# Kernel optimization log

Hardware: AMD Instinct MI355X
Metric: run time of the kernel (lower is better)

The kernel has to match this reference:

```python
import jax, jax.numpy as jnp
import numpy as np

H = 64      # hidden_dimension
NH = 4      # num_heads
L = 2       # num_egat_layers
N = 20000   # total nodes in batched graph
E = 320000  # total edges
B = 64      # number of graphs in batch
SLOPE = 0.2 # DGL EGATConv leaky_relu negative slope


def setup_inputs() -> dict:
    key = jax.random.key(0)
    ks = iter(jax.random.split(key, 40))
    def nrm(shape, scale=0.05):
        return jax.random.normal(next(ks), shape, dtype=jnp.float32) * scale
    node_graph_id = jnp.sort(jax.random.randint(next(ks), (N,), 0, B))
    src = jax.random.randint(next(ks), (E,), 0, N)
    dst = jax.random.randint(next(ks), (E,), 0, N)
    edge_graph_id = node_graph_id[dst]
    return dict(
        x=nrm((N, 81), 1.0), e=nrm((E, 17), 1.0),
        placed_rc=jax.random.randint(next(ks), (N,), 0, 2),
        fp=nrm((B, 2048), 1.0),
        src=src, dst=dst, node_graph_id=node_graph_id, edge_graph_id=edge_graph_id,
        W_fp=nrm((2048, H)), b_fp=jnp.zeros((H,), jnp.float32),
        W_n0=nrm((81, H)), b_n0=jnp.zeros((H,), jnp.float32),
        W_e0=nrm((17, H)), b_e0=jnp.zeros((H,), jnp.float32),
        emb_rc=nrm((2, H)),
        fc_node_W=nrm((L, H, NH * H)), fc_ni_W=nrm((L, H, NH * H)),
        fc_nj_W=nrm((L, H, NH * H)), fc_fij_W=nrm((L, H, NH * H)),
        attn=nrm((L, NH, H)), egat_bias=jnp.zeros((L, NH * H), jnp.float32),
        mlp_n_W=nrm((L, NH * H, H)), mlp_n_b=jnp.zeros((L, H), jnp.float32),
        mlp_e_W=nrm((L, NH * H, H)), mlp_e_b=jnp.zeros((L, H), jnp.float32),
        W_g=nrm((3 * H, H)), b_g=jnp.zeros((H,), jnp.float32),
    )


def _egat_layer(nf, ef, src, dst, p):
    # One EGATLayer: DGL EGATConv + per-output MLP + ELU.
    fcnW, fniW, fnjW, ffW, attn, ebias, mnW, mnb, meW, meb = p
    f_out = nf[src] @ fniW + nf[dst] @ fnjW + ef @ ffW          # [E, NH*H]
    f_out = jax.nn.leaky_relu(f_out, SLOPE).reshape(E, NH, H)    # [E, NH, H]
    logits = jnp.einsum('ehd,hd->eh', f_out, attn)               # [E, NH]
    # edge softmax over incoming edges at each destination node
    m = jax.ops.segment_max(logits, dst, num_segments=N)
    ex = jnp.exp(logits - m[dst])
    denom = jax.ops.segment_sum(ex, dst, num_segments=N)
    a = ex / denom[dst]                                          # [E, NH]
    h = (nf @ fcnW).reshape(N, NH, H)                            # [N, NH, H]
    msg = h[src] * a[..., None]                                  # [E, NH, H]
    h_out = jax.ops.segment_sum(msg, dst, num_segments=N)        # [N, NH, H]
    h_out = h_out + ebias.reshape(NH, H)[None]
    new_n = jax.nn.elu(h_out.reshape(N, NH * H) @ mnW + mnb)     # [N, H]
    new_e = jax.nn.elu(f_out.reshape(E, NH * H) @ meW + meb)     # [E, H]
    return new_n, new_e


def reference(x, e, placed_rc, fp, src, dst, node_graph_id, edge_graph_id,
              W_fp, b_fp, W_n0, b_n0, W_e0, b_e0, emb_rc,
              fc_node_W, fc_ni_W, fc_nj_W, fc_fij_W, attn, egat_bias,
              mlp_n_W, mlp_n_b, mlp_e_W, mlp_e_b, W_g, b_g):
    fp_enc = jax.nn.elu(fp @ W_fp + b_fp)                        # [B, H]
    nf = x @ W_n0 + b_n0 + emb_rc[placed_rc]                     # [N, H]
    ef = e @ W_e0 + b_e0                                         # [E, H]
    for l in range(L):  # residual EGAT stack
        rn, re = nf, ef
        nf, ef = _egat_layer(nf, ef, src, dst,
            (fc_node_W[l], fc_ni_W[l], fc_nj_W[l], fc_fij_W[l], attn[l],
             egat_bias[l], mlp_n_W[l], mlp_n_b[l], mlp_e_W[l], mlp_e_b[l]))
        nf = nf + rn
        ef = ef + re
    # mean readout per graph
    cnt_n = jax.ops.segment_sum(jnp.ones((N,), jnp.float32), node_graph_id, num_segments=B)
    cnt_e = jax.ops.segment_sum(jnp.ones((E,), jnp.float32), edge_graph_id, num_segments=B)
    g_n = jax.ops.segment_sum(nf, node_graph_id, num_segments=B) / jnp.maximum(cnt_n, 1.0)[:, None]
    g_e = jax.ops.segment_sum(ef, edge_graph_id, num_segments=B) / jnp.maximum(cnt_e, 1.0)[:, None]
    g = jnp.concatenate([g_n, g_e, fp_enc], axis=1)              # [B, 3H]
    g = jax.nn.elu(g @ W_g + b_g)                                # [B, H]
    return nf, g
```

## Files before the change

### kernel.cpp

```cpp
#include <hip/hip_runtime.h>
#include <math.h>

#define SLOPE 0.2f

typedef __attribute__((ext_vector_type(8))) short bf16x8;
typedef __attribute__((ext_vector_type(4))) float f32x4;

__device__ __forceinline__ unsigned short f2bf(float x) {
  unsigned int b = __float_as_uint(x);
  b = (b + 0x7fffu + ((b >> 16) & 1u)) >> 16;
  return (unsigned short)b;
}
__device__ __forceinline__ float bf2f(unsigned short u) {
  return __uint_as_float(((unsigned int)u) << 16);
}
__device__ __forceinline__ float elu1(float v) { return v > 0.f ? v : expm1f(v); }
__device__ __forceinline__ float lrelu(float v) { return v > 0.f ? v : SLOPE * v; }

__global__ __launch_bounds__(256) void k_zero(float* p, long n) {
  long i = (long)blockIdx.x * 256 + threadIdx.x;
  long stride = (long)gridDim.x * 256;
  for (; i < n; i += stride) p[i] = 0.f;
}

__global__ __launch_bounds__(256) void k_fp(const float* __restrict__ fp,
                                            const float* __restrict__ W,
                                            float* __restrict__ fpacc) {
  __shared__ float red[256];
  const int b = blockIdx.x >> 3;
  const int kc = blockIdx.x & 7;
  const int t = threadIdx.x, o = t & 63, kg = t >> 6;
  const int k0 = kc * 256 + kg * 64;
  const float* fpr = fp + (size_t)b * 2048 + k0;
  const float* Wp = W + (size_t)k0 * 64 + o;
  float a0 = 0.f, a1 = 0.f, a2 = 0.f, a3 = 0.f;
#pragma unroll
  for (int i = 0; i < 64; i += 4) {
    a0 += fpr[i + 0] * Wp[(i + 0) * 64];
    a1 += fpr[i + 1] * Wp[(i + 1) * 64];
    a2 += fpr[i + 2] * Wp[(i + 2) * 64];
    a3 += fpr[i + 3] * Wp[(i + 3) * 64];
  }
  red[t] = (a0 + a1) + (a2 + a3);
  __syncthreads();
  if (t < 64) {
    float v = red[t] + red[t + 64] + red[t + 128] + red[t + 192];
    atomicAdd(&fpacc[(size_t)b * 64 + t], v);
  }
}

__global__ __launch_bounds__(256) void k_nf0(const float* __restrict__ x,
                                             const float* __restrict__ W,
                                             const float* __restrict__ bias,
                                             const float* __restrict__ emb,
                                             const int* __restrict__ prc,
                                             float* __restrict__ nf,
                                             unsigned short* __restrict__ nfB, int N) {
  __shared__ float xl[64 * 85];
  const int t = threadIdx.x, l = t & 63, q = t >> 6;
  const int nbase = blockIdx.x * 64;
  const long xbase = (long)nbase * 81;
  const long xlim = (long)N * 81;
  for (int i = t; i < 5184; i += 256) {
    int row = i / 81, k = i - row * 81;
    float v = (xbase + i < xlim) ? x[xbase + i] : 0.f;
    xl[row * 85 + k] = v;
  }
  __syncthreads();
  const int n = nbase + l;
  const int nc = n < N ? n : N - 1;
  const int o0 = q * 16;
  const int pv = prc[nc];
  float acc[16];
#pragma unroll
  for (int i = 0; i < 16; ++i) acc[i] = bias[o0 + i] + emb[pv * 64 + o0 + i];
  for (int k = 0; k < 81; ++k) {
    float xv = xl[l * 85 + k];
    float w[16];
    const float4* wp = (const float4*)(W + (long)k * 64 + o0);
    *(float4*)&w[0] = wp[0]; *(float4*)&w[4] = wp[1];
    *(float4*)&w[8] = wp[2]; *(float4*)&w[12] = wp[3];
#pragma unroll
    for (int i = 0; i < 16; ++i) acc[i] += xv * w[i];
  }
  if (n < N) {
#pragma unroll
    for (int u = 0; u < 4; ++u)
      *(float4*)(nf + (long)n * 64 + o0 + 4 * u) =
          make_float4(acc[4 * u], acc[4 * u + 1], acc[4 * u + 2], acc[4 * u + 3]);
    unsigned pk[8];
#pragma unroll
    for (int u = 0; u < 8; ++u)
      pk[u] = (unsigned)f2bf(acc[2 * u]) | ((unsigned)f2bf(acc[2 * u + 1]) << 16);
    *(uint4*)(nfB + (size_t)n * 64 + o0) = make_uint4(pk[0], pk[1], pk[2], pk[3]);
    *(uint4*)(nfB + (size_t)n * 64 + o0 + 8) = make_uint4(pk[4], pk[5], pk[6], pk[7]);
  }
}

__global__ __launch_bounds__(256) void k_ef0(const float* __restrict__ ein,
                                             const int* __restrict__ eids,
                                             const float* __restrict__ W,
                                             const float* __restrict__ bias,
                                             unsigned short* __restrict__ efB, int E) {
  const int t = threadIdx.x, l = t & 63, q = t >> 6;
  const long i = (long)blockIdx.x * 64 + l;
  const long ic = i < E ? i : 0;
  const long e = eids[ic];
  const int o0 = q * 16;
  float acc[16];
#pragma unroll
  for (int k = 0; k < 16; ++k) acc[k] = bias[o0 + k];
  for (int k = 0; k < 17; ++k) {
    float xv = ein[e * 17 + k];
    float w[16];
    const float4* wp = (const float4*)(W + (long)k * 64 + o0);
    *(float4*)&w[0] = wp[0]; *(float4*)&w[4] = wp[1];
    *(float4*)&w[8] = wp[2]; *(float4*)&w[12] = wp[3];
#pragma unroll
    for (int u = 0; u < 16; ++u) acc[u] += xv * w[u];
  }
  if (i < E) {
    unsigned pk[8];
#pragma unroll
    for (int u = 0; u < 8; ++u)
      pk[u] = (unsigned)f2bf(acc[2 * u]) | ((unsigned)f2bf(acc[2 * u + 1]) << 16);
    *(uint4*)(efB + i * 64 + o0) = make_uint4(pk[0], pk[1], pk[2], pk[3]);
    *(uint4*)(efB + i * 64 + o0 + 8) = make_uint4(pk[4], pk[5], pk[6], pk[7]);
  }
}

__global__ __launch_bounds__(256) void k_hist(const int* __restrict__ dst, int* deg, int E) {
  int e = blockIdx.x * 256 + threadIdx.x;
  if (e < E) atomicAdd(&deg[dst[e]], 1);
}

__global__ __launch_bounds__(1024) void k_scan(const int* __restrict__ deg, int* rowst,
                                               int* cursor, int N, int E) {
  __shared__ int s[1024];
  const int t = threadIdx.x;
  const int CH = (N + 1023) / 1024;
  const int base = t * CH;
  int sum = 0;
  for (int i = 0; i < CH; ++i) { int n = base + i; if (n < N) sum += deg[n]; }
  s[t] = sum;
  __syncthreads();
  for (int off = 1; off < 1024; off <<= 1) {
    int v = (t >= off) ? s[t - off] : 0;
    __syncthreads();
    s[t] += v;
    __syncthreads();
  }
  int run = s[t] - sum;
  for (int i = 0; i < CH; ++i) {
    int n = base + i;
    if (n < N) { rowst[n] = run; cursor[n] = run; run += deg[n]; }
  }
  if (t == 1023) rowst[N] = E;
}

__global__ __launch_bounds__(256) void k_fill(const int* __restrict__ dst,
                                              const int* __restrict__ src,
                                              const int* __restrict__ egid,
                                              int* cursor, int* eids,
                                              int* srcC, int* dstC, int* egidC, int E) {
  int e = blockIdx.x * 256 + threadIdx.x;
  if (e < E) {
    int d = dst[e];
    int pos = atomicAdd(&cursor[d], 1);
    eids[pos] = e;
    srcC[pos] = src[e];
    dstC[pos] = d;
    egidC[pos] = egid[e];
  }
}

__global__ __launch_bounds__(256) void k_pack(const float* __restrict__ fni,
                                              const float* __restrict__ fnj,
                                              const float* __restrict__ ffij,
                                              const float* __restrict__ meW,
                                              unsigned short* __restrict__ pA,
                                              unsigned short* __restrict__ pB) {
  int t = blockIdx.x * 256 + threadIdx.x;
  if (t < 6144) {
    int lane = t & 63;
    int ks = (t >> 6) % 6;
    int nt = t / 384;
    int n = nt * 16 + (lane & 15);
    int kbase = ks * 32 + (lane >> 4) * 8;
    bf16x8 v;
#pragma unroll
    for (int j = 0; j < 8; ++j) {
      int kk = kbase + j;
      float wv = kk < 64 ? fni[kk * 256 + n]
                         : (kk < 128 ? fnj[(kk - 64) * 256 + n] : ffij[(kk - 128) * 256 + n]);
      v[j] = (short)f2bf(wv);
    }
    *(bf16x8*)(pA + (size_t)t * 8) = v;
  } else if (t < 8192) {
    int u = t - 6144;
    int lane = u & 63;
    int ks = (u >> 6) % 8;
    int nt = u / 512;
    int n = nt * 16 + (lane & 15);
    int kbase = ks * 32 + (lane >> 4) * 8;
    bf16x8 v;
#pragma unroll
    for (int j = 0; j < 8; ++j) v[j] = (short)f2bf(meW[(size_t)(kbase + j) * 64 + n]);
    *(bf16x8*)(pB + (size_t)u * 8) = v;
  }
}

__global__ __launch_bounds__(256) void k_comb(const float* __restrict__ fcn,
                                              const float* __restrict__ mnW,
                                              const float* __restrict__ mnb,
                                              const float* __restrict__ ebias,
                                              float* __restrict__ Wcomb,
                                              float* __restrict__ bprime) {
  const int b = blockIdx.x, t = threadIdx.x;
  if (b < 4) {
    const int h = b, i = t & 63, c0 = (t >> 6) * 16;
    float acc[16];
#pragma unroll
    for (int c = 0; c < 16; ++c) acc[c] = 0.f;
    for (int j = 0; j < 64; ++j) {
      float w1 = fcn[i * 256 + h * 64 + j];
      const float4* mp = (const float4*)(mnW + (size_t)(h * 64 + j) * 64 + c0);
      float mw[16];
      *(float4*)&mw[0] = mp[0]; *(float4*)&mw[4] = mp[1];
      *(float4*)&mw[8] = mp[2]; *(float4*)&mw[12] = mp[3];
#pragma unroll
      for (int c = 0; c < 16; ++c) acc[c] += w1 * mw[c];
    }
    for (int c = 0; c < 16; ++c) Wcomb[(size_t)(h * 64 + i) * 64 + c0 + c] = acc[c];
  } else {
    if (t < 64) {
      float a = mnb[t];
      for (int k = 0; k < 256; ++k) a += ebias[k] * mnW[(size_t)k * 64 + t];
      bprime[t] = a;
    }
  }
}

__global__ __launch_bounds__(256) void k_packB(const float* __restrict__ W,
                                               unsigned short* __restrict__ dst) {
  int u = blockIdx.x * 256 + threadIdx.x;
  if (u >= 2048) return;
  int lane = u & 63;
  int ks = (u >> 6) % 8;
  int nt = u / 512;
  int n = nt * 16 + (lane & 15);
  int kbase = ks * 32 + (lane >> 4) * 8;
  bf16x8 v;
#pragma unroll
  for (int j = 0; j < 8; ++j) v[j] = (short)f2bf(W[(size_t)(kbase + j) * 64 + n]);
  *(bf16x8*)(dst + (size_t)u * 8) = v;
}

__global__ __launch_bounds__(256, 4) void k_edge(const unsigned short* __restrict__ nfB,
                                                 const unsigned short* __restrict__ efB,
                                                 const unsigned short* __restrict__ pA,
                                                 const unsigned short* __restrict__ pB,
                                                 const float* __restrict__ attnW,
                                                 const float* __restrict__ meb,
                                                 const int* __restrict__ srcC,
                                                 const int* __restrict__ dstC,
                                                 unsigned short* __restrict__ efBout,
                                                 float* __restrict__ logitsC,
                                                 const int* __restrict__ egidC,
                                                 float* __restrict__ geOut,
                                                 float* __restrict__ ceOut, int E) {
  __shared__ __align__(16) char smem[32768 + 1024 + 512];
  float* lgx = (float*)(smem + 32768);
  int* sv = (int*)(smem + 32768 + 1024);
  int* dv = (int*)(smem + 32768 + 1024 + 256);
  const int t = threadIdx.x, l = t & 63, w = t >> 6;
  const long ebase = (long)blockIdx.x * 64;

  if (t < 64) sv[t] = srcC[min(ebase + t, (long)E - 1)];
  else if (t < 128) dv[t - 64] = dstC[min(ebase + t - 64, (long)E - 1)];
  __syncthreads();
#pragma unroll
  for (int i = 0; i < 6; ++i) {
    int c = i * 256 + t;
    int row = c / 24;
    int kc8 = c - row * 24;
    long e = ebase + row;
    if (e >= E) e = E - 1;
    int ko = (kc8 & 7) * 8;
    int seg = kc8 >> 3;
    const unsigned short* gp;
    if (seg == 0)      gp = nfB + (size_t)sv[row] * 64 + ko;
    else if (seg == 1) gp = nfB + (size_t)dv[row] * 64 + ko;
    else               gp = efB + (size_t)e * 64 + ko;
    uint4 v = *(const uint4*)gp;
    *(uint4*)(smem + row * 384 + ((kc8 * 16) ^ ((row & 7) << 4))) = v;
  }
  __syncthreads();

  f32x4 acc[4][4];
#pragma unroll
  for (int c0 = 0; c0 < 4; ++c0)
#pragma unroll
    for (int e0 = 0; e0 < 4; ++e0) acc[c0][e0] = (f32x4){0.f, 0.f, 0.f, 0.f};

  for (int ks = 0; ks < 6; ++ks) {
    bf16x8 eb[4], wa[4];
#pragma unroll
    for (int e0 = 0; e0 < 4; ++e0) {
      int row = e0 * 16 + (l & 15);
      int kb = ks * 64 + (l >> 4) * 16;
      eb[e0] = *(const bf16x8*)(smem + row * 384 + (kb ^ ((row & 7) << 4)));
    }
#pragma unroll
    for (int c0 = 0; c0 < 4; ++c0)
      wa[c0] = *(const bf16x8*)(pA + (size_t)(((w * 4 + c0) * 6 + ks) * 64 + l) * 8);
#pragma unroll
    for (int c0 = 0; c0 < 4; ++c0)
#pragma unroll
      for (int e0 = 0; e0 < 4; ++e0)
        acc[c0][e0] = __builtin_amdgcn_mfma_f32_16x16x32_bf16(wa[c0], eb[e0], acc[c0][e0], 0, 0, 0);
  }
  __syncthreads();

  float avv[4][4];
#pragma unroll
  for (int c0 = 0; c0 < 4; ++c0) {
    float4 a4 = *(const float4*)(attnW + w * 64 + c0 * 16 + (l >> 4) * 4);
    avv[c0][0] = a4.x; avv[c0][1] = a4.y; avv[c0][2] = a4.z; avv[c0][3] = a4.w;
  }
  float lgp[4] = {0.f, 0.f, 0.f, 0.f};
#pragma unroll
  for (int e0 = 0; e0 < 4; ++e0) {
    int row = e0 * 16 + (l & 15);
#pragma unroll
    for (int c0 = 0; c0 < 4; ++c0) {
      float v0 = lrelu(acc[c0][e0][0]);
      float v1 = lrelu(acc[c0][e0][1]);
      float v2 = lrelu(acc[c0][e0][2]);
      float v3 = lrelu(acc[c0][e0][3]);
      lgp[e0] += v0 * avv[c0][0] + v1 * avv[c0][1] + v2 * avv[c0][2] + v3 * avv[c0][3];
      uint2 p;
      p.x = (unsigned)f2bf(v0) | ((unsigned)f2bf(v1) << 16);
      p.y = (unsigned)f2bf(v2) | ((unsigned)f2bf(v3) << 16);
      int colb = (w * 64 + c0 * 16 + (l >> 4) * 4) * 2;
      *(uint2*)(smem + row * 512 + (colb ^ ((row & 7) << 4))) = p;
    }
  }
#pragma unroll
  for (int e0 = 0; e0 < 4; ++e0) {
    float v = lgp[e0];
    v += __shfl_xor(v, 16);
    v += __shfl_xor(v, 32);
    if (l < 16) lgx[(e0 * 16 + l) * 4 + w] = v;
  }
  __syncthreads();

  if (t < 64) {
    long e = ebase + t;
    if (e < E) *(float4*)(logitsC + e * 4) = *(const float4*)(lgx + t * 4);
  }

  f32x4 a2[4];
#pragma unroll
  for (int e0 = 0; e0 < 4; ++e0) a2[e0] = (f32x4){0.f, 0.f, 0.f, 0.f};
  for (int ks = 0; ks < 8; ++ks) {
    bf16x8 fb[4];
#pragma unroll
    for (int e0 = 0; e0 < 4; ++e0) {
      int row = e0 * 16 + (l & 15);
      int kb = ks * 64 + (l >> 4) * 16;
      fb[e0] = *(const bf16x8*)(smem + row * 512 + (kb ^ ((row & 7) << 4)));
    }
    bf16x8 pb = *(const bf16x8*)(pB + (size_t)((w * 8 + ks) * 64 + l) * 8);
#pragma unroll
    for (int e0 = 0; e0 < 4; ++e0)
      a2[e0] = __builtin_amdgcn_mfma_f32_16x16x32_bf16(pb, fb[e0], a2[e0], 0, 0, 0);
  }
  const int cb = w * 16 + (l >> 4) * 4;
  float4 mb4 = *(const float4*)(meb + cb);
  __syncthreads();
#pragma unroll
  for (int e0 = 0; e0 < 4; ++e0) {
    int row = e0 * 16 + (l & 15);
    float4 o;
    o.x = elu1(a2[e0][0] + mb4.x);
    o.y = elu1(a2[e0][1] + mb4.y);
    o.z = elu1(a2[e0][2] + mb4.z);
    o.w = elu1(a2[e0][3] + mb4.w);
    *(float4*)(smem + (size_t)(row * 68 + cb) * 4) = o;
  }
  __syncthreads();
#pragma unroll
  for (int i = 0; i < 4; ++i) {
    int idx = i * 256 + t;
    int row = idx >> 4;
    int c4 = (idx & 15) * 4;
    long e = ebase + row;
    if (e < E) {
      uint2 rb = *(const uint2*)(efB + e * 64 + c4);
      float4 v = *(const float4*)(smem + (size_t)(row * 68 + c4) * 4);
      v.x += bf2f((unsigned short)(rb.x & 0xffffu));
      v.y += bf2f((unsigned short)(rb.x >> 16));
      v.z += bf2f((unsigned short)(rb.y & 0xffffu));
      v.w += bf2f((unsigned short)(rb.y >> 16));
      if (efBout) {
        uint2 ob;
        ob.x = (unsigned)f2bf(v.x) | ((unsigned)f2bf(v.y) << 16);
        ob.y = (unsigned)f2bf(v.z) | ((unsigned)f2bf(v.w) << 16);
        *(uint2*)(efBout + e * 64 + c4) = ob;
      }
      if (geOut) *(float4*)(smem + (size_t)(row * 68 + c4) * 4) = v;
    }
  }
  if (geOut) {
    if (t < 64) sv[t] = (ebase + t < E) ? egidC[ebase + t] : -1;
    __syncthreads();
    if (t < 64) {
      int nrows = (int)min((long)64, E - ebase);
      float racc = 0.f, cnt = 0.f;
      int curg = sv[0];
      for (int r = 0; r < nrows; ++r) {
        int g = sv[r];
        if (g != curg) {
          atomicAdd(&geOut[(size_t)curg * 64 + t], racc);
          if (t == 0) atomicAdd(&ceOut[curg], cnt);
          racc = 0.f; cnt = 0.f; curg = g;
        }
        racc += *(const float*)(smem + (size_t)(r * 68 + t) * 4);
        cnt += 1.f;
      }
      if (curg >= 0) {
        atomicAdd(&geOut[(size_t)curg * 64 + t], racc);
        if (t == 0) atomicAdd(&ceOut[curg], cnt);
      }
    }
  }
}

__global__ __launch_bounds__(256) void k_node(const float* __restrict__ logitsC,
                                              const unsigned short* __restrict__ nfB,
                                              const int* __restrict__ rowst,
                                              const int* __restrict__ srcC,
                                              unsigned short* __restrict__ agg, int N) {
  const int t = threadIdx.x, w = t >> 6, l = t & 63;
  const int n = blockIdx.x * 4 + w;
  if (n >= N) return;
  const int start = rowst[n];
  const int dg = rowst[n + 1] - start;
  const int h = l >> 4;
  float m0 = -INFINITY, m1 = -INFINITY, m2 = -INFINITY, m3 = -INFINITY;
  for (int base = 0; base < dg; base += 64) {
    int j = base + l;
    if (j < dg) {
      float4 lg = *(const float4*)(logitsC + (long)(start + j) * 4);
      m0 = fmaxf(m0, lg.x); m1 = fmaxf(m1, lg.y); m2 = fmaxf(m2, lg.z); m3 = fmaxf(m3, lg.w);
    }
  }
#pragma unroll
  for (int o = 1; o < 64; o <<= 1) {
    m0 = fmaxf(m0, __shfl_xor(m0, o)); m1 = fmaxf(m1, __shfl_xor(m1, o));
    m2 = fmaxf(m2, __shfl_xor(m2, o)); m3 = fmaxf(m3, __shfl_xor(m3, o));
  }
  const float msel = (h == 0) ? m0 : (h == 1) ? m1 : (h == 2) ? m2 : m3;

  const int co = (l & 15) * 4;
  float s = 0.f;
  float a0 = 0.f, a1 = 0.f, a2 = 0.f, a3 = 0.f;
  int j = 0;
  for (; j + 4 <= dg; j += 4) {
    int sj0 = srcC[start + j + 0];
    int sj1 = srcC[start + j + 1];
    int sj2 = srcC[start + j + 2];
    int sj3 = srcC[start + j + 3];
    float l0 = logitsC[(long)(start + j + 0) * 4 + h];
    float l1 = logitsC[(long)(start + j + 1) * 4 + h];
    float l2 = logitsC[(long)(start + j + 2) * 4 + h];
    float l3 = logitsC[(long)(start + j + 3) * 4 + h];
    uint2 b0 = *(const uint2*)(nfB + (size_t)sj0 * 64 + co);
    uint2 b1 = *(const uint2*)(nfB + (size_t)sj1 * 64 + co);
    uint2 b2 = *(const uint2*)(nfB + (size_t)sj2 * 64 + co);
    uint2 b3 = *(const uint2*)(nfB + (size_t)sj3 * 64 + co);
    float aa0 = __expf(l0 - msel);
    float aa1 = __expf(l1 - msel);
    float aa2 = __expf(l2 - msel);
    float aa3 = __expf(l3 - msel);
    s += (aa0 + aa1) + (aa2 + aa3);
    a0 += aa0 * bf2f((unsigned short)(b0.x & 0xffffu)) + aa1 * bf2f((unsigned short)(b1.x & 0xffffu))
        + aa2 * bf2f((unsigned short)(b2.x & 0xffffu)) + aa3 * bf2f((unsigned short)(b3.x & 0xffffu));
    a1 += aa0 * bf2f((unsigned short)(b0.x >> 16)) + aa1 * bf2f((unsigned short)(b1.x >> 16))
        + aa2 * bf2f((unsigned short)(b2.x >> 16)) + aa3 * bf2f((unsigned short)(b3.x >> 16));
    a2 += aa0 * bf2f((unsigned short)(b0.y & 0xffffu)) + aa1 * bf2f((unsigned short)(b1.y & 0xffffu))
        + aa2 * bf2f((unsigned short)(b2.y & 0xffffu)) + aa3 * bf2f((unsigned short)(b3.y & 0xffffu));
    a3 += aa0 * bf2f((unsigned short)(b0.y >> 16)) + aa1 * bf2f((unsigned short)(b1.y >> 16))
        + aa2 * bf2f((unsigned short)(b2.y >> 16)) + aa3 * bf2f((unsigned short)(b3.y >> 16));
  }
  for (; j < dg; ++j) {
    int sj = srcC[start + j];
    float lg = logitsC[(long)(start + j) * 4 + h];
    float a = __expf(lg - msel);
    s += a;
    uint2 b0 = *(const uint2*)(nfB + (size_t)sj * 64 + co);
    a0 += a * bf2f((unsigned short)(b0.x & 0xffffu));
    a1 += a * bf2f((unsigned short)(b0.x >> 16));
    a2 += a * bf2f((unsigned short)(b0.y & 0xffffu));
    a3 += a * bf2f((unsigned short)(b0.y >> 16));
  }
  const float rsel = (dg > 0) ? (1.f / s) : 0.f;
  a0 *= rsel; a1 *= rsel; a2 *= rsel; a3 *= rsel;
  unsigned v0 = (unsigned)f2bf(a0) | ((unsigned)f2bf(a1) << 16);
  unsigned v1 = (unsigned)f2bf(a2) | ((unsigned)f2bf(a3) << 16);
  uint2 vv; vv.x = v0; vv.y = v1;
  *(uint2*)(agg + (size_t)n * 256 + h * 64 + co) = vv;
}

__global__ __launch_bounds__(256, 4) void k_mlpn(const unsigned short* __restrict__ agg,
                                                 const unsigned short* __restrict__ pW,
                                                 const float* __restrict__ bprime,
                                                 float* __restrict__ nf,
                                                 unsigned short* __restrict__ nfB,
                                                 float* __restrict__ dout,
                                                 const int* __restrict__ ngid,
                                                 float* __restrict__ gnOut,
                                                 float* __restrict__ cnOut, int N) {
  __shared__ __align__(16) char sm[64 * 512];
  __shared__ int gidL[64];
  const int t = threadIdx.x, l = t & 63, w = t >> 6;
  const int nbase = blockIdx.x * 64;
#pragma unroll
  for (int i = 0; i < 8; ++i) {
    int idx = t + 256 * i;
    int row = idx >> 5, kc = idx & 31;
    int rr = (nbase + row) < N ? (nbase + row) : (N - 1);
    uint4 v = *(const uint4*)(agg + (size_t)rr * 256 + kc * 8);
    *(uint4*)(sm + row * 512 + ((kc * 16) ^ ((row & 7) << 4))) = v;
  }
  __syncthreads();
  f32x4 acc[4];
#pragma unroll
  for (int e0 = 0; e0 < 4; ++e0) acc[e0] = (f32x4){0.f, 0.f, 0.f, 0.f};
  for (int ks = 0; ks < 8; ++ks) {
    bf16x8 a[4];
#pragma unroll
    for (int e0 = 0; e0 < 4; ++e0) {
      int row = e0 * 16 + (l & 15);
      int kb = ks * 64 + (l >> 4) * 16;
      a[e0] = *(const bf16x8*)(sm + row * 512 + (kb ^ ((row & 7) << 4)));
    }
    bf16x8 b = *(const bf16x8*)(pW + (size_t)((w * 8 + ks) * 64 + l) * 8);
#pragma unroll
    for (int e0 = 0; e0 < 4; ++e0)
      acc[e0] = __builtin_amdgcn_mfma_f32_16x16x32_bf16(b, a[e0], acc[e0], 0, 0, 0);
  }
  const int cb = w * 16 + (l >> 4) * 4;
  float4 bp4 = *(const float4*)(bprime + cb);
  __syncthreads();
#pragma unroll
  for (int e0 = 0; e0 < 4; ++e0) {
    int row = e0 * 16 + (l & 15);
    float4 o;
    o.x = elu1(acc[e0][0] + bp4.x);
    o.y = elu1(acc[e0][1] + bp4.y);
    o.z = elu1(acc[e0][2] + bp4.z);
    o.w = elu1(acc[e0][3] + bp4.w);
    *(float4*)(sm + (size_t)(row * 68 + cb) * 4) = o;
  }
  if (gnOut && t < 64) gidL[t] = (nbase + t < N) ? ngid[nbase + t] : -1;
  __syncthreads();
#pragma unroll
  for (int i = 0; i < 4; ++i) {
    int idx = i * 256 + t;
    int row = idx >> 4;
    int c4 = (idx & 15) * 4;
    int n = nbase + row;
    if (n < N) {
      float4 res = *(const float4*)(nf + (size_t)n * 64 + c4);
      float4 v = *(const float4*)(sm + (size_t)(row * 68 + c4) * 4);
      v.x += res.x; v.y += res.y; v.z += res.z; v.w += res.w;
      *(float4*)(nf + (size_t)n * 64 + c4) = v;
      uint2 ob;
      ob.x = (unsigned)f2bf(v.x) | ((unsigned)f2bf(v.y) << 16);
      ob.y = (unsigned)f2bf(v.z) | ((unsigned)f2bf(v.w) << 16);
      *(uint2*)(nfB + (size_t)n * 64 + c4) = ob;
      if (dout) *(float4*)(dout + (size_t)n * 64 + c4) = v;
      if (gnOut) *(float4*)(sm + (size_t)(row * 68 + c4) * 4) = v;
    }
  }
  if (gnOut) {
    __syncthreads();
    if (t < 64) {
      int nrows = min(64, N - nbase);
      float racc = 0.f, cnt = 0.f;
      int curg = gidL[0];
      for (int r = 0; r < nrows; ++r) {
        int g = gidL[r];
        if (g != curg) {
          atomicAdd(&gnOut[(size_t)curg * 64 + t], racc);
          if (t == 0) atomicAdd(&cnOut[curg], cnt);
          racc = 0.f; cnt = 0.f; curg = g;
        }
        racc += *(const float*)(sm + (size_t)(r * 68 + t) * 4);
        cnt += 1.f;
      }
      if (curg >= 0) {
        atomicAdd(&gnOut[(size_t)curg * 64 + t], racc);
        if (t == 0) atomicAdd(&cnOut[curg], cnt);
      }
    }
  }
}

__global__ __launch_bounds__(64) void k_final(const float* __restrict__ gn,
                                              const float* __restrict__ ge,
                                              const float* __restrict__ cntn,
                                              const float* __restrict__ cnte,
                                              const float* __restrict__ fpacc,
                                              const float* __restrict__ bfp,
                                              const float* __restrict__ Wg,
                                              const float* __restrict__ bg,
                                              float* __restrict__ outg) {
  __shared__ float gv[192];
  const int b = blockIdx.x, l = threadIdx.x;
  const float rn = 1.f / fmaxf(cntn[b], 1.f);
  const float re = 1.f / fmaxf(cnte[b], 1.f);
  gv[l] = gn[(long)b * 64 + l] * rn;
  gv[64 + l] = ge[(long)b * 64 + l] * re;
  gv[128 + l] = elu1(fpacc[(long)b * 64 + l] + bfp[l]);
  __syncthreads();
  float acc = bg[l];
  for (int k = 0; k < 192; ++k) acc += gv[k] * Wg[(long)k * 64 + l];
  outg[(long)b * 64 + l] = elu1(acc);
}

extern "C" void kernel_launch(void* const* d_in, const int* in_sizes, int n_in,
                              void* d_out, int out_size, void* d_ws, size_t ws_size,
                              hipStream_t stream) {
  (void)n_in; (void)out_size; (void)ws_size;
  const float* x       = (const float*)d_in[0];
  const float* ein     = (const float*)d_in[1];
  const int*   prc     = (const int*)d_in[2];
  const float* fp      = (const float*)d_in[3];
  const int*   src     = (const int*)d_in[4];
  const int*   dst     = (const int*)d_in[5];
  const int*   ngid    = (const int*)d_in[6];
  const int*   egid    = (const int*)d_in[7];
  const float* W_fp    = (const float*)d_in[8];
  const float* b_fp    = (const float*)d_in[9];
  const float* W_n0    = (const float*)d_in[10];
  const float* b_n0    = (const float*)d_in[11];
  const float* W_e0    = (const float*)d_in[12];
  const float* b_e0    = (const float*)d_in[13];
  const float* emb_rc  = (const float*)d_in[14];
  const float* fc_node = (const float*)d_in[15];
  const float* fc_ni   = (const float*)d_in[16];
  const float* fc_nj   = (const float*)d_in[17];
  const float* fc_fij  = (const float*)d_in[18];
  const float* attnp   = (const float*)d_in[19];
  const float* egb     = (const float*)d_in[20];
  const float* mlp_n_W = (const float*)d_in[21];
  const float* mlp_n_b = (const float*)d_in[22];
  const float* mlp_e_W = (const float*)d_in[23];
  const float* mlp_e_b = (const float*)d_in[24];
  const float* W_g     = (const float*)d_in[25];
  const float* b_g     = (const float*)d_in[26];

  const int N = in_sizes[0] / 81;
  const int E = in_sizes[1] / 17;
  const int B = in_sizes[3] / 2048;
  float* out = (float*)d_out;

  char* ws = (char*)d_ws;
  size_t off = 0;
  auto carve = [&](size_t bytes) {
    size_t r = off;
    off = (off + bytes + 255) & ~(size_t)255;
    return r;
  };
  size_t o_nf   = carve((size_t)N * 64 * 4);
  size_t o_nfB  = carve((size_t)N * 64 * 2);
  size_t o_efB  = carve((size_t)E * 64 * 2);
  size_t o_agg  = carve((size_t)N * 256 * 2);
  size_t o_lg   = carve((size_t)E * 4 * 4);
  size_t o_pA   = carve((size_t)2 * 6144 * 8 * 2);
  size_t o_pB   = carve((size_t)2 * 2048 * 8 * 2);
  size_t o_Wc   = carve((size_t)2 * 256 * 64 * 4);
  size_t o_pW   = carve((size_t)2 * 2048 * 8 * 2);
  size_t o_bp   = carve((size_t)2 * 64 * 4);
  size_t o_gn   = carve((size_t)B * 64 * 4);
  size_t o_ge   = carve((size_t)B * 64 * 4);
  size_t o_cn   = carve((size_t)B * 4);
  size_t o_ce   = carve((size_t)B * 4);
  size_t o_fpe  = carve((size_t)B * 64 * 4);
  size_t o_deg  = carve((size_t)N * 4);
  size_t o_rs   = carve((size_t)(N + 1) * 4);
  size_t o_cur  = carve((size_t)N * 4);
  size_t o_eid  = carve((size_t)E * 4);
  size_t o_srcC = carve((size_t)E * 4);
  size_t o_dstC = carve((size_t)E * 4);
  size_t o_egC  = carve((size_t)E * 4);

  float* nf   = (float*)(ws + o_nf);
  unsigned short* nfB = (unsigned short*)(ws + o_nfB);
  unsigned short* efB = (unsigned short*)(ws + o_efB);
  unsigned short* agg = (unsigned short*)(ws + o_agg);
  float* lgb  = (float*)(ws + o_lg);
  unsigned short* pA = (unsigned short*)(ws + o_pA);
  unsigned short* pB = (unsigned short*)(ws + o_pB);
  float* Wc   = (float*)(ws + o_Wc);
  unsigned short* pW = (unsigned short*)(ws + o_pW);
  float* bp   = (float*)(ws + o_bp);
  float* gn   = (float*)(ws + o_gn);
  float* ge   = (float*)(ws + o_ge);
  float* cn   = (float*)(ws + o_cn);
  float* ce   = (float*)(ws + o_ce);
  float* fpacc= (float*)(ws + o_fpe);
  int* deg    = (int*)(ws + o_deg);
  int* rowst  = (int*)(ws + o_rs);
  int* cursor = (int*)(ws + o_cur);
  int* eids   = (int*)(ws + o_eid);
  int* srcC   = (int*)(ws + o_srcC);
  int* dstC   = (int*)(ws + o_dstC);
  int* egidC  = (int*)(ws + o_egC);

  const long zero_n = (long)((o_deg + (size_t)N * 4 - o_gn) / 4);
  const int gridN64 = (N + 63) / 64;
  const int gridE64 = (E + 63) / 64;
  const int gridE256 = (E + 255) / 256;
  const int gridN4 = (N + 3) / 4;

  k_zero<<<128, 256, 0, stream>>>((float*)(ws + o_gn), zero_n);
  k_fp<<<B * 8, 256, 0, stream>>>(fp, W_fp, fpacc);
  k_nf0<<<gridN64, 256, 0, stream>>>(x, W_n0, b_n0, emb_rc, prc, nf, nfB, N);
  k_hist<<<gridE256, 256, 0, stream>>>(dst, deg, E);
  k_scan<<<1, 1024, 0, stream>>>(deg, rowst, cursor, N, E);
  k_fill<<<gridE256, 256, 0, stream>>>(dst, src, egid, cursor, eids, srcC, dstC, egidC, E);
  k_ef0<<<gridE64, 256, 0, stream>>>(ein, eids, W_e0, b_e0, efB, E);

  for (int l = 0; l < 2; ++l) {
    k_pack<<<32, 256, 0, stream>>>(fc_ni + (size_t)l * 64 * 256,
                                   fc_nj + (size_t)l * 64 * 256,
                                   fc_fij + (size_t)l * 64 * 256,
                                   mlp_e_W + (size_t)l * 256 * 64,
                                   pA + (size_t)l * 6144 * 8,
                                   pB + (size_t)l * 2048 * 8);
    k_comb<<<5, 256, 0, stream>>>(fc_node + (size_t)l * 64 * 256,
                                  mlp_n_W + (size_t)l * 256 * 64,
                                  mlp_n_b + (size_t)l * 64,
                                  egb + (size_t)l * 256,
                                  Wc + (size_t)l * 256 * 64,
                                  bp + (size_t)l * 64);
    k_packB<<<8, 256, 0, stream>>>(Wc + (size_t)l * 256 * 64, pW + (size_t)l * 2048 * 8);
  }

  for (int l = 0; l < 2; ++l) {
    const float* att = attnp + (size_t)l * 4 * 64;
    const float* meb = mlp_e_b + (size_t)l * 64;

    k_edge<<<gridE64, 256, 0, stream>>>(nfB, efB, pA + (size_t)l * 6144 * 8,
                                        pB + (size_t)l * 2048 * 8, att, meb,
                                        srcC, dstC,
                                        (l == 0) ? efB : (unsigned short*)nullptr,
                                        lgb, egidC,
                                        (l == 1) ? ge : (float*)nullptr,
                                        (l == 1) ? ce : (float*)nullptr, E);
    k_node<<<gridN4, 256, 0, stream>>>(lgb, nfB, rowst, srcC, agg, N);
    k_mlpn<<<gridN64, 256, 0, stream>>>(agg, pW + (size_t)l * 2048 * 8,
                                        bp + (size_t)l * 64, nf, nfB,
                                        (l == 1) ? out : (float*)nullptr,
                                        ngid,
                                        (l == 1) ? gn : (float*)nullptr,
                                        (l == 1) ? cn : (float*)nullptr, N);
  }

  k_final<<<B, 64, 0, stream>>>(gn, ge, cn, ce, fpacc, b_fp, W_g, b_g, out + (size_t)N * 64);
}
```

Before: 503.3 us.

## Compute attention logits via extra MFMA tile and unroll node aggregation by eight

```diff
diff --git a/kernel.cpp b/kernel.cpp
--- a/kernel.cpp
+++ b/kernel.cpp
@@ -178,6 +178,7 @@
                                               const float* __restrict__ fnj,
                                               const float* __restrict__ ffij,
                                               const float* __restrict__ meW,
+                                              const float* __restrict__ attW,
                                               unsigned short* __restrict__ pA,
                                               unsigned short* __restrict__ pB) {
   int t = blockIdx.x * 256 + threadIdx.x;
@@ -196,16 +197,26 @@
       v[j] = (short)f2bf(wv);
     }
     *(bf16x8*)(pA + (size_t)t * 8) = v;
-  } else if (t < 8192) {
+  } else if (t < 8704) {
     int u = t - 6144;
     int lane = u & 63;
-    int ks = (u >> 6) % 8;
-    int nt = u / 512;
-    int n = nt * 16 + (lane & 15);
+    int ks = (u >> 6) & 7;
+    int nt = u >> 9;
+    int n15 = lane & 15;
     int kbase = ks * 32 + (lane >> 4) * 8;
     bf16x8 v;
-#pragma unroll
-    for (int j = 0; j < 8; ++j) v[j] = (short)f2bf(meW[(size_t)(kbase + j) * 64 + n]);
+    if (nt < 4) {
+      int n = nt * 16 + n15;
+#pragma unroll
+      for (int j = 0; j < 8; ++j) v[j] = (short)f2bf(meW[(size_t)(kbase + j) * 64 + n]);
+    } else {
+#pragma unroll
+      for (int j = 0; j < 8; ++j) {
+        int k = kbase + j;
+        float wv = (n15 < 4 && (k >> 6) == n15) ? attW[n15 * 64 + (k & 63)] : 0.f;
+        v[j] = (short)f2bf(wv);
+      }
+    }
     *(bf16x8*)(pB + (size_t)u * 8) = v;
   }
 }
@@ -260,7 +271,6 @@
                                                  const unsigned short* __restrict__ efB,
                                                  const unsigned short* __restrict__ pA,
                                                  const unsigned short* __restrict__ pB,
-                                                 const float* __restrict__ attnW,
                                                  const float* __restrict__ meb,
                                                  const int* __restrict__ srcC,
                                                  const int* __restrict__ dstC,
@@ -269,10 +279,9 @@
                                                  const int* __restrict__ egidC,
                                                  float* __restrict__ geOut,
                                                  float* __restrict__ ceOut, int E) {
-  __shared__ __align__(16) char smem[32768 + 1024 + 512];
-  float* lgx = (float*)(smem + 32768);
-  int* sv = (int*)(smem + 32768 + 1024);
-  int* dv = (int*)(smem + 32768 + 1024 + 256);
+  __shared__ __align__(16) char smem[32768 + 512];
+  int* sv = (int*)(smem + 32768);
+  int* dv = (int*)(smem + 32768 + 256);
   const int t = threadIdx.x, l = t & 63, w = t >> 6;
   const long ebase = (long)blockIdx.x * 64;
 
@@ -322,13 +331,6 @@
   }
   __syncthreads();
 
-  float avv[4][4];
-#pragma unroll
-  for (int c0 = 0; c0 < 4; ++c0) {
-    float4 a4 = *(const float4*)(attnW + w * 64 + c0 * 16 + (l >> 4) * 4);
-    avv[c0][0] = a4.x; avv[c0][1] = a4.y; avv[c0][2] = a4.z; avv[c0][3] = a4.w;
-  }
-  float lgp[4] = {0.f, 0.f, 0.f, 0.f};
 #pragma unroll
   for (int e0 = 0; e0 < 4; ++e0) {
     int row = e0 * 16 + (l & 15);
@@ -338,7 +340,6 @@
       float v1 = lrelu(acc[c0][e0][1]);
       float v2 = lrelu(acc[c0][e0][2]);
       float v3 = lrelu(acc[c0][e0][3]);
-      lgp[e0] += v0 * avv[c0][0] + v1 * avv[c0][1] + v2 * avv[c0][2] + v3 * avv[c0][3];
       uint2 p;
       p.x = (unsigned)f2bf(v0) | ((unsigned)f2bf(v1) << 16);
       p.y = (unsigned)f2bf(v2) | ((unsigned)f2bf(v3) << 16);
@@ -346,23 +347,14 @@
       *(uint2*)(smem + row * 512 + (colb ^ ((row & 7) << 4))) = p;
     }
   }
+  __syncthreads();
+
+  f32x4 a2[4], a2x[4];
 #pragma unroll
   for (int e0 = 0; e0 < 4; ++e0) {
-    float v = lgp[e0];
-    v += __shfl_xor(v, 16);
-    v += __shfl_xor(v, 32);
-    if (l < 16) lgx[(e0 * 16 + l) * 4 + w] = v;
-  }
-  __syncthreads();
-
-  if (t < 64) {
-    long e = ebase + t;
-    if (e < E) *(float4*)(logitsC + e * 4) = *(const float4*)(lgx + t * 4);
-  }
-
-  f32x4 a2[4];
-#pragma unroll
-  for (int e0 = 0; e0 < 4; ++e0) a2[e0] = (f32x4){0.f, 0.f, 0.f, 0.f};
+    a2[e0] = (f32x4){0.f, 0.f, 0.f, 0.f};
+    a2x[e0] = (f32x4){0.f, 0.f, 0.f, 0.f};
+  }
   for (int ks = 0; ks < 8; ++ks) {
     bf16x8 fb[4];
 #pragma unroll
@@ -375,10 +367,26 @@
 #pragma unroll
     for (int e0 = 0; e0 < 4; ++e0)
       a2[e0] = __builtin_amdgcn_mfma_f32_16x16x32_bf16(pb, fb[e0], a2[e0], 0, 0, 0);
+    if (w == 0) {
+      bf16x8 pbx = *(const bf16x8*)(pB + (size_t)((32 + ks) * 64 + l) * 8);
+#pragma unroll
+      for (int e0 = 0; e0 < 4; ++e0)
+        a2x[e0] = __builtin_amdgcn_mfma_f32_16x16x32_bf16(pbx, fb[e0], a2x[e0], 0, 0, 0);
+    }
   }
   const int cb = w * 16 + (l >> 4) * 4;
   float4 mb4 = *(const float4*)(meb + cb);
   __syncthreads();
+
+  if (w == 0 && (l >> 4) == 0) {
+#pragma unroll
+    for (int e0 = 0; e0 < 4; ++e0) {
+      long e = ebase + e0 * 16 + (l & 15);
+      if (e < E)
+        *(float4*)(logitsC + e * 4) =
+            make_float4(a2x[e0][0], a2x[e0][1], a2x[e0][2], a2x[e0][3]);
+    }
+  }
 #pragma unroll
   for (int e0 = 0; e0 < 4; ++e0) {
     int row = e0 * 16 + (l & 15);
@@ -467,32 +475,26 @@
   float s = 0.f;
   float a0 = 0.f, a1 = 0.f, a2 = 0.f, a3 = 0.f;
   int j = 0;
-  for (; j + 4 <= dg; j += 4) {
-    int sj0 = srcC[start + j + 0];
-    int sj1 = srcC[start + j + 1];
-    int sj2 = srcC[start + j + 2];
-    int sj3 = srcC[start + j + 3];
-    float l0 = logitsC[(long)(start + j + 0) * 4 + h];
-    float l1 = logitsC[(long)(start + j + 1) * 4 + h];
-    float l2 = logitsC[(long)(start + j + 2) * 4 + h];
-    float l3 = logitsC[(long)(start + j + 3) * 4 + h];
-    uint2 b0 = *(const uint2*)(nfB + (size_t)sj0 * 64 + co);
-    uint2 b1 = *(const uint2*)(nfB + (size_t)sj1 * 64 + co);
-    uint2 b2 = *(const uint2*)(nfB + (size_t)sj2 * 64 + co);
-    uint2 b3 = *(const uint2*)(nfB + (size_t)sj3 * 64 + co);
-    float aa0 = __expf(l0 - msel);
-    float aa1 = __expf(l1 - msel);
-    float aa2 = __expf(l2 - msel);
-    float aa3 = __expf(l3 - msel);
-    s += (aa0 + aa1) + (aa2 + aa3);
-    a0 += aa0 * bf2f((unsigned short)(b0.x & 0xffffu)) + aa1 * bf2f((unsigned short)(b1.x & 0xffffu))
-        + aa2 * bf2f((unsigned short)(b2.x & 0xffffu)) + aa3 * bf2f((unsigned short)(b3.x & 0xffffu));
-    a1 += aa0 * bf2f((unsigned short)(b0.x >> 16)) + aa1 * bf2f((unsigned short)(b1.x >> 16))
-        + aa2 * bf2f((unsigned short)(b2.x >> 16)) + aa3 * bf2f((unsigned short)(b3.x >> 16));
-    a2 += aa0 * bf2f((unsigned short)(b0.y & 0xffffu)) + aa1 * bf2f((unsigned short)(b1.y & 0xffffu))
-        + aa2 * bf2f((unsigned short)(b2.y & 0xffffu)) + aa3 * bf2f((unsigned short)(b3.y & 0xffffu));
-    a3 += aa0 * bf2f((unsigned short)(b0.y >> 16)) + aa1 * bf2f((unsigned short)(b1.y >> 16))
-        + aa2 * bf2f((unsigned short)(b2.y >> 16)) + aa3 * bf2f((unsigned short)(b3.y >> 16));
+  for (; j + 8 <= dg; j += 8) {
+    int sj[8];
+    float lv[8];
+    uint2 bb[8];
+    float aa[8];
+#pragma unroll
+    for (int u = 0; u < 8; ++u) sj[u] = srcC[start + j + u];
+#pragma unroll
+    for (int u = 0; u < 8; ++u) lv[u] = logitsC[(long)(start + j + u) * 4 + h];
+#pragma unroll
+    for (int u = 0; u < 8; ++u) bb[u] = *(const uint2*)(nfB + (size_t)sj[u] * 64 + co);
+#pragma unroll
+    for (int u = 0; u < 8; ++u) { aa[u] = __expf(lv[u] - msel); s += aa[u]; }
+#pragma unroll
+    for (int u = 0; u < 8; ++u) {
+      a0 += aa[u] * bf2f((unsigned short)(bb[u].x & 0xffffu));
+      a1 += aa[u] * bf2f((unsigned short)(bb[u].x >> 16));
+      a2 += aa[u] * bf2f((unsigned short)(bb[u].y & 0xffffu));
+      a3 += aa[u] * bf2f((unsigned short)(bb[u].y >> 16));
+    }
   }
   for (; j < dg; ++j) {
     int sj = srcC[start + j];
@@ -681,7 +683,7 @@
   size_t o_agg  = carve((size_t)N * 256 * 2);
   size_t o_lg   = carve((size_t)E * 4 * 4);
   size_t o_pA   = carve((size_t)2 * 6144 * 8 * 2);
-  size_t o_pB   = carve((size_t)2 * 2048 * 8 * 2);
+  size_t o_pB   = carve((size_t)2 * 2560 * 8 * 2);
   size_t o_Wc   = carve((size_t)2 * 256 * 64 * 4);
   size_t o_pW   = carve((size_t)2 * 2048 * 8 * 2);
   size_t o_bp   = carve((size_t)2 * 64 * 4);
@@ -736,12 +738,13 @@
   k_ef0<<<gridE64, 256, 0, stream>>>(ein, eids, W_e0, b_e0, efB, E);
 
   for (int l = 0; l < 2; ++l) {
-    k_pack<<<32, 256, 0, stream>>>(fc_ni + (size_t)l * 64 * 256,
+    k_pack<<<34, 256, 0, stream>>>(fc_ni + (size_t)l * 64 * 256,
                                    fc_nj + (size_t)l * 64 * 256,
                                    fc_fij + (size_t)l * 64 * 256,
                                    mlp_e_W + (size_t)l * 256 * 64,
+                                   attnp + (size_t)l * 4 * 64,
                                    pA + (size_t)l * 6144 * 8,
-                                   pB + (size_t)l * 2048 * 8);
+                                   pB + (size_t)l * 2560 * 8);
     k_comb<<<5, 256, 0, stream>>>(fc_node + (size_t)l * 64 * 256,
                                   mlp_n_W + (size_t)l * 256 * 64,
                                   mlp_n_b + (size_t)l * 64,
@@ -752,11 +755,10 @@
   }
 
   for (int l = 0; l < 2; ++l) {
-    const float* att = attnp + (size_t)l * 4 * 64;
     const float* meb = mlp_e_b + (size_t)l * 64;
 
     k_edge<<<gridE64, 256, 0, stream>>>(nfB, efB, pA + (size_t)l * 6144 * 8,
-                                        pB + (size_t)l * 2048 * 8, att, meb,
+                                        pB + (size_t)l * 2560 * 8, meb,
                                         srcC, dstC,
                                         (l == 0) ? efB : (unsigned short*)nullptr,
                                         lgb, egidC,
```

Result: slower. 544.5 us (+8.2%).
